# Kernel tuning notes

Measured on AMD Instinct MI355X. Metric: run time of the kernel, lower is better.

Reference implementation:

```python
import jax, jax.numpy as jnp
import numpy as np

D = 256; H = 8; L = 4; K = 4; AS = 2; HD = D // H
KK = K * K
LEVEL_SHAPES = [(128, 128), (64, 64), (32, 32), (16, 16)]


def _kernel_indices():
    # kernel_size=4 (even): linspace(-1.5, 1.5, 4); stack [j, i] then / K
    idx = jnp.linspace(-1.5, 1.5, K)
    ii, jj = jnp.meshgrid(idx, idx, indexing='ij')
    return jnp.stack([jj, ii], axis=-1).reshape(-1, 2) / K  # (KK, 2)


def _bilinear(vf, g, Hl, Wl):
    # vf: (b, H, Hl*Wl, HD) per-level value; g: (b, l1, H, KK, 2) in [0,1]
    # grid_sample semantics, align_corners=False, zero padding
    b, l1, h, kk, _ = g.shape
    x = g[..., 0] * Wl - 0.5
    y = g[..., 1] * Hl - 0.5
    x0 = jnp.floor(x)
    y0 = jnp.floor(y)
    acc = None
    for dx, dy in ((0, 0), (1, 0), (0, 1), (1, 1)):
        xi = x0 + dx
        yi = y0 + dy
        w = (1.0 - jnp.abs(x - xi)) * (1.0 - jnp.abs(y - yi))
        valid = (xi >= 0) & (xi < Wl) & (yi >= 0) & (yi < Hl)
        idx = (jnp.clip(yi, 0, Hl - 1) * Wl + jnp.clip(xi, 0, Wl - 1)).astype(jnp.int32)
        idx = idx.transpose(0, 2, 1, 3).reshape(b, h, l1 * kk)
        gth = jnp.take_along_axis(vf, idx[..., None], axis=2)  # (b,H,l1*kk,HD)
        ww = (w * valid).transpose(0, 2, 1, 3).reshape(b, h, l1 * kk)
        c = gth * ww[..., None]
        acc = c if acc is None else acc + c
    return acc.reshape(b, h, l1, kk, HD).transpose(0, 2, 1, 3, 4)  # (b,l1,H,kk,HD)


def setup_inputs() -> dict:
    key = jax.random.key(0)
    ks = jax.random.split(key, 9)
    b, l1 = 4, 1024
    l2 = sum(h * w for h, w in LEVEL_SHAPES)  # 21760
    query = jax.random.normal(ks[0], (b, l1, D), jnp.float32)
    value = jax.random.normal(ks[1], (b, l2, D), jnp.float32)
    centers = jax.random.uniform(ks[2], (b, l1, 2), jnp.float32)
    sizes = jax.random.uniform(ks[3], (b, l1, 2), jnp.float32) * 0.2 + 0.05
    ref_windows = jnp.concatenate([centers, sizes], axis=-1)  # (b,l1,4) cx,cy,w,h
    s = 1.0 / np.sqrt(D)
    Wv = jax.random.normal(ks[4], (D, D), jnp.float32) * s
    bv = jnp.zeros((D,), jnp.float32)
    Wo = jax.random.normal(ks[5], (D, D), jnp.float32) * s
    bo = jnp.zeros((D,), jnp.float32)
    Wbox = jax.random.normal(ks[6], (L * H * 4, D), jnp.float32) * 0.01
    bbox = jax.random.uniform(ks[7], (H * L * 4,), jnp.float32)
    Wattn = jax.random.normal(ks[8], (H * L * AS * AS, D), jnp.float32) * s
    battn = jnp.zeros((H * L * AS * AS,), jnp.float32)
    v_shape = np.array(LEVEL_SHAPES, np.int64)
    starts = np.cumsum([0] + [h * w for h, w in LEVEL_SHAPES[:-1]])
    v_start_index = np.array(starts, np.int64)
    v_mask = jnp.zeros((b, l2), bool)
    return dict(query=query, value=value, ref_windows=ref_windows, Wv=Wv, bv=bv,
                Wo=Wo, bo=bo, Wbox=Wbox, bbox=bbox, Wattn=Wattn, battn=battn,
                v_shape=v_shape, v_start_index=v_start_index, v_mask=v_mask)


def reference(query, value, ref_windows, Wv, bv, Wo, bo, Wbox, bbox, Wattn, battn,
              v_shape, v_start_index, v_mask):
    b, l1, _ = query.shape
    l2 = value.shape[1]
    # value projection + padding mask
    v = value @ Wv.T + bv
    v = jnp.where(v_mask[..., None], 0.0, v).reshape(b, l2, H, HD)
    # where to attend: offset boxes -> sampling grid (normalizer=None branch)
    off = (query @ Wbox.T + bbox).reshape(b, l1, H, L, 4)
    refw = ref_windows[:, :, None, None, :]            # (b,l1,1,1,4)
    refsz = jnp.concatenate([refw[..., 2:4], refw[..., 2:4]], axis=-1)
    boxes = refw + off / 8.0 * refsz                   # (b,l1,H,L,4)
    center = boxes[..., None, :2]
    size = boxes[..., None, 2:]
    grid = center + _kernel_indices() * jax.nn.relu(size)  # (b,l1,H,L,KK,2)
    # attention weights (attn_size grid upsampled to kernel_size by repeat_interleave)
    aw = (query @ Wattn.T + battn).reshape(b, l1, H, L, AS, AS)
    nr = K // AS
    aw = jnp.repeat(jnp.repeat(aw, nr, axis=-1), nr, axis=-2)  # (b,l1,H,L,K,K)
    sw = jax.nn.softmax(aw.reshape(b, l1, H, -1), axis=-1).reshape(b, l1, H, L, KK)
    lw = jax.nn.softmax(aw, axis=3).reshape(b, l1, H, L, KK)
    out = jnp.zeros((b, l1, H, HD), query.dtype)
    mout = jnp.zeros((b, l1, H, HD), query.dtype)
    for li in range(L):
        Hl, Wl = int(v_shape[li, 0]), int(v_shape[li, 1])
        st = int(v_start_index[li])
        vf = v[:, st:st + Hl * Wl].transpose(0, 2, 1, 3)  # (b,H,Hl*Wl,HD)
        samp = _bilinear(vf, grid[:, :, :, li], Hl, Wl)   # (b,l1,H,KK,HD)
        out = out + jnp.einsum('bqhkd,bqhk->bqhd', samp, sw[:, :, :, li])
        mout = mout + jnp.einsum('bqhkd,bqhk->bqhd', samp, lw[:, :, :, li])
    out = out.reshape(b, l1, D) @ Wo.T + bo
    mout = mout.reshape(b, l1, D) @ Wo.T + bo
    return out, mout, aw
```

## Files before the change

### kernel.cpp

```cpp
#include <hip/hip_runtime.h>
#include <hip/hip_bf16.h>


typedef __attribute__((ext_vector_type(8))) short short8;
typedef __attribute__((ext_vector_type(4))) float f32x4;
typedef __attribute__((ext_vector_type(4))) unsigned int uint4v;

__device__ __forceinline__ unsigned short f2bf(float f) {
    unsigned int u = __float_as_uint(f);
    unsigned int r = u + 0x7FFFu + ((u >> 16) & 1u);
    return (unsigned short)(r >> 16);
}
__device__ __forceinline__ unsigned int pkbf(float a, float b) {
    __hip_bfloat162 h = __float22bfloat162_rn(float2{a, b});
    return *reinterpret_cast<unsigned int*>(&h);
}
__device__ __forceinline__ short8 pack2(float4 x, float4 y) {
    uint4v u;
    u[0] = pkbf(x.x, x.y); u[1] = pkbf(x.z, x.w);
    u[2] = pkbf(y.x, y.y); u[3] = pkbf(y.z, y.w);
    return __builtin_bit_cast(short8, u);
}

__device__ __forceinline__ void storeC(float* C, size_t i, float v) { C[i] = v; }
__device__ __forceinline__ void storeC(unsigned short* C, size_t i, float v) { C[i] = f2bf(v); }

template <typename OutT>
__device__ __forceinline__ void gemm_body3(
    const float* __restrict__ A, const float* __restrict__ W,
    const float* __restrict__ bias, OutT* __restrict__ C,
    int N, int bm, int bn, char* smem)
{
    const int tid  = threadIdx.x;
    const int lane = tid & 63;
    const int wave = tid >> 6;
    const int wm = (wave & 1) * 64;
    const int wn = (wave >> 1) * 64;
    const int kg = lane >> 4;
    const int lm = lane & 15;

    char* ldsA = smem;
    char* ldsW = smem + 16384;

    f32x4 acc[4][4];
#pragma unroll
    for (int i = 0; i < 4; ++i)
#pragma unroll
        for (int j = 0; j < 4; ++j) {
            acc[i][j][0] = 0.f; acc[i][j][1] = 0.f;
            acc[i][j][2] = 0.f; acc[i][j][3] = 0.f;
        }

    const int prow = tid >> 1;
    const int ph   = tid & 1;
    const float* Ag = A + (size_t)(bm + prow) * 256 + ph * 16;
    const float* Wg = W + (size_t)(bn + prow) * 256 + ph * 16;
    const int f   = (prow >> 1) & 3;
    const int pp  = ph ^ (f >> 1);
    const int wlo = (f & 1) * 16;
    const int whi = wlo ^ 16;
    char* wA = ldsA + prow * 64 + pp * 32;
    char* wW = ldsW + prow * 64 + pp * 32;

    const int aslot = (kg ^ ((lm >> 1) & 3)) * 16;
    const int aoff  = (wm + lm) * 64 + aslot;
    const int woff  = (wn + lm) * 64 + aslot;

    float4 fa[4], fw[4];
#define ISSUE_VQ(K0)                                          \
    {                                                         \
        _Pragma("unroll")                                     \
        for (int q = 0; q < 4; ++q) {                         \
            fa[q] = *(const float4*)(Ag + (K0) + 4 * q);      \
            fw[q] = *(const float4*)(Wg + (K0) + 4 * q);      \
        }                                                     \
    }

    ISSUE_VQ(0)

    for (int it = 0; it < 8; ++it) {
        const int b = it & 1;
        char* wAb = wA + b * 8192;
        char* wWb = wW + b * 8192;
        *(short8*)(wAb + wlo) = pack2(fa[0], fa[1]);
        *(short8*)(wAb + whi) = pack2(fa[2], fa[3]);
        *(short8*)(wWb + wlo) = pack2(fw[0], fw[1]);
        *(short8*)(wWb + whi) = pack2(fw[2], fw[3]);
        __syncthreads();
        if (it < 7) ISSUE_VQ(32 * (it + 1))
        const char* bA = ldsA + b * 8192;
        const char* bW = ldsW + b * 8192;
        short8 af[4];
#pragma unroll
        for (int i = 0; i < 4; ++i)
            af[i] = *(const short8*)(bA + aoff + i * 1024);
#pragma unroll
        for (int j = 0; j < 4; ++j) {
            short8 bf = *(const short8*)(bW + woff + j * 1024);
#pragma unroll
            for (int i = 0; i < 4; ++i)
                acc[i][j] = __builtin_amdgcn_mfma_f32_16x16x32_bf16(
                    af[i], bf, acc[i][j], 0, 0, 0);
        }
    }
#undef ISSUE_VQ

#pragma unroll
    for (int j = 0; j < 4; ++j) {
        int col = bn + wn + j * 16 + lm;
        float bcol = bias[col];
#pragma unroll
        for (int i = 0; i < 4; ++i) {
#pragma unroll
            for (int r = 0; r < 4; ++r) {
                int row = bm + wm + i * 16 + kg * 4 + r;
                storeC(C, (size_t)row * N + col, acc[i][j][r] + bcol);
            }
        }
    }
}

#define LDA 56

__device__ __forceinline__ void gemm_body_f32(
    const float* __restrict__ A, const float* __restrict__ W,
    const float* __restrict__ bias, float* __restrict__ C,
    int N, int bm, int bn, unsigned short* As, unsigned short* Ws)
{
    const int tid  = threadIdx.x;
    const int lane = tid & 63;
    const int wave = tid >> 6;
    const int wm = (wave & 1) * 64;
    const int wn = (wave >> 1) * 64;
    const int lr = tid >> 1;
    const int lh = (tid & 1) * 16;
    const int kg = lane >> 4;
    const int lm = lane & 15;

    f32x4 acc[4][4];
#pragma unroll
    for (int i = 0; i < 4; ++i)
#pragma unroll
        for (int j = 0; j < 4; ++j) {
            acc[i][j][0] = 0.f; acc[i][j][1] = 0.f;
            acc[i][j][2] = 0.f; acc[i][j][3] = 0.f;
        }

    const float* Ap = A + (size_t)(bm + lr) * 256 + lh;
    const float* Wp = W + (size_t)(bn + lr) * 256 + lh;
    unsigned short* Asp = &As[lr * LDA + lh];
    unsigned short* Wsp = &Ws[lr * LDA + lh];

    for (int k0 = 0; k0 < 256; k0 += 32) {
        float4 a0 = *(const float4*)(Ap + k0);
        float4 a1 = *(const float4*)(Ap + k0 + 4);
        float4 a2 = *(const float4*)(Ap + k0 + 8);
        float4 a3 = *(const float4*)(Ap + k0 + 12);
        float4 w0 = *(const float4*)(Wp + k0);
        float4 w1 = *(const float4*)(Wp + k0 + 4);
        float4 w2 = *(const float4*)(Wp + k0 + 8);
        float4 w3 = *(const float4*)(Wp + k0 + 12);
        __syncthreads();
        *(short8*)(Asp)     = pack2(a0, a1);
        *(short8*)(Asp + 8) = pack2(a2, a3);
        *(short8*)(Wsp)     = pack2(w0, w1);
        *(short8*)(Wsp + 8) = pack2(w2, w3);
        __syncthreads();
        short8 af[4], bfr[4];
#pragma unroll
        for (int i = 0; i < 4; ++i)
            af[i] = *(const short8*)&As[(wm + i * 16 + lm) * LDA + kg * 8];
#pragma unroll
        for (int j = 0; j < 4; ++j)
            bfr[j] = *(const short8*)&Ws[(wn + j * 16 + lm) * LDA + kg * 8];
#pragma unroll
        for (int i = 0; i < 4; ++i)
#pragma unroll
            for (int j = 0; j < 4; ++j)
                acc[i][j] = __builtin_amdgcn_mfma_f32_16x16x32_bf16(
                    af[i], bfr[j], acc[i][j], 0, 0, 0);
    }

#pragma unroll
    for (int j = 0; j < 4; ++j) {
        int col = bn + wn + j * 16 + lm;
        float bcol = bias[col];
#pragma unroll
        for (int i = 0; i < 4; ++i)
#pragma unroll
            for (int r = 0; r < 4; ++r) {
                int row = bm + wm + i * 16 + kg * 4 + r;
                C[(size_t)row * N + col] = acc[i][j][r] + bcol;
            }
    }
}

__device__ __forceinline__ void gemm_body_bf16A(
    const unsigned short* __restrict__ A, const float* __restrict__ W,
    const float* __restrict__ bias, float* __restrict__ C,
    int N, int bm, int bn, unsigned short* As, unsigned short* Ws)
{
    const int tid  = threadIdx.x;
    const int lane = tid & 63;
    const int wave = tid >> 6;
    const int wm = (wave & 1) * 64;
    const int wn = (wave >> 1) * 64;
    const int lr = tid >> 1;
    const int lh = (tid & 1) * 16;
    const int kg = lane >> 4;
    const int lm = lane & 15;

    f32x4 acc[4][4];
#pragma unroll
    for (int i = 0; i < 4; ++i)
#pragma unroll
        for (int j = 0; j < 4; ++j) {
            acc[i][j][0] = 0.f; acc[i][j][1] = 0.f;
            acc[i][j][2] = 0.f; acc[i][j][3] = 0.f;
        }

    const unsigned short* Ap = A + (size_t)(bm + lr) * 256 + lh;
    const float* Wp = W + (size_t)(bn + lr) * 256 + lh;
    unsigned short* Asp = &As[lr * LDA + lh];
    unsigned short* Wsp = &Ws[lr * LDA + lh];

    for (int k0 = 0; k0 < 256; k0 += 32) {
        uint4v a01 = *(const uint4v*)(Ap + k0);
        uint4v a23 = *(const uint4v*)(Ap + k0 + 8);
        float4 w0 = *(const float4*)(Wp + k0);
        float4 w1 = *(const float4*)(Wp + k0 + 4);
        float4 w2 = *(const float4*)(Wp + k0 + 8);
        float4 w3 = *(const float4*)(Wp + k0 + 12);
        __syncthreads();
        *(short8*)(Asp)     = __builtin_bit_cast(short8, a01);
        *(short8*)(Asp + 8) = __builtin_bit_cast(short8, a23);
        *(short8*)(Wsp)     = pack2(w0, w1);
        *(short8*)(Wsp + 8) = pack2(w2, w3);
        __syncthreads();
        short8 af[4], bfr[4];
#pragma unroll
        for (int i = 0; i < 4; ++i)
            af[i] = *(const short8*)&As[(wm + i * 16 + lm) * LDA + kg * 8];
#pragma unroll
        for (int j = 0; j < 4; ++j)
            bfr[j] = *(const short8*)&Ws[(wn + j * 16 + lm) * LDA + kg * 8];
#pragma unroll
        for (int i = 0; i < 4; ++i)
#pragma unroll
            for (int j = 0; j < 4; ++j)
                acc[i][j] = __builtin_amdgcn_mfma_f32_16x16x32_bf16(
                    af[i], bfr[j], acc[i][j], 0, 0, 0);
    }

#pragma unroll
    for (int j = 0; j < 4; ++j) {
        int col = bn + wn + j * 16 + lm;
        float bcol = bias[col];
#pragma unroll
        for (int i = 0; i < 4; ++i)
#pragma unroll
            for (int r = 0; r < 4; ++r) {
                int row = bm + wm + i * 16 + kg * 4 + r;
                C[(size_t)row * N + col] = acc[i][j][r] + bcol;
            }
    }
}

__global__ __launch_bounds__(256, 4) void gemm_vq_kernel(
    const float* __restrict__ value, const float* __restrict__ Wv,
    const float* __restrict__ bv, unsigned short* __restrict__ v,
    const float* __restrict__ query,
    const float* __restrict__ Wbox, const float* __restrict__ bbox, float* __restrict__ off,
    const float* __restrict__ Wattn, const float* __restrict__ battn, float* __restrict__ awr)
{
    __shared__ __align__(16) char smem[32768];
    const int x = blockIdx.x;
    if (x < 1360) {
        gemm_body3<unsigned short>(value, Wv, bv, v, 256,
                                   (x >> 1) * 128, (x & 1) * 128, smem);
    } else {
        const int idx = x - 1360;
        const int bm = (idx & 31) * 128;
        unsigned short* As = (unsigned short*)smem;
        unsigned short* Ws = As + 128 * LDA;
        if (idx < 32) gemm_body_f32(query, Wbox, bbox, off, 128, bm, 0, As, Ws);
        else          gemm_body_f32(query, Wattn, battn, awr, 128, bm, 0, As, Ws);
    }
}

__global__ __launch_bounds__(256) void gemm_o_kernel(
    const unsigned short* __restrict__ A, const float* __restrict__ W,
    const float* __restrict__ bias, float* __restrict__ C)
{
    __shared__ __align__(16) unsigned short As[128 * LDA];
    __shared__ __align__(16) unsigned short Ws[128 * LDA];
    gemm_body_bf16A(A, W, bias, C, 256, blockIdx.x * 128, blockIdx.y * 128, As, Ws);
}

__global__ __launch_bounds__(512, 8) void sample_kernel(
    const unsigned short* __restrict__ v, const float* __restrict__ off,
    const float* __restrict__ awr, const float* __restrict__ refw,
    float* __restrict__ aw_out, unsigned short* __restrict__ accb)
{
    const int x  = blockIdx.x;
    const int bq = ((x & 3) << 10) | (x >> 2);
    const int b  = bq >> 10;
    const int t  = threadIdx.x;

    __shared__ float ref4[4];
    __shared__ float awl[128];
    __shared__ float bxs[128];
    __shared__ float swl[512];
    __shared__ float lwl[512];
    __shared__ int4  tp[32 * 66];

    if (t < 4)   ref4[t] = refw[bq * 4 + t];
    if (t < 128) awl[t] = awr[(size_t)bq * 128 + t];
    __syncthreads();

    if (t < 128) {
        float o = off[(size_t)bq * 128 + t];
        int comp = t & 3;
        float r0 = ref4[0], r1 = ref4[1], r2 = ref4[2], r3 = ref4[3];
        float bx;
        if (comp == 0)      bx = r0 + o * 0.125f * r2;
        else if (comp == 1) bx = r1 + o * 0.125f * r3;
        else if (comp == 2) bx = r2 + o * 0.125f * r2;
        else                bx = r3 + o * 0.125f * r3;
        bxs[t] = bx;

        const int h = t >> 4, r = t & 15;
        float a = awl[t];
        float m = a;
#pragma unroll
        for (int s = 1; s < 16; s <<= 1) m = fmaxf(m, __shfl_xor(m, s, 16));
        float se = expf(a - m);
#pragma unroll
        for (int s = 1; s < 16; s <<= 1) se += __shfl_xor(se, s, 16);
        const float inv_s = 1.0f / (4.0f * se);

        float* awq = aw_out + (size_t)bq * 512 + h * 64;
#pragma unroll
        for (int j = 0; j < 4; ++j) {
            int eidx = r * 4 + j;
            int l  = eidx >> 4;
            int ky = (eidx >> 2) & 3;
            int kx = eidx & 3;
            int pos = (ky >> 1) * 2 + (kx >> 1);
            float raw = awl[h * 16 + l * 4 + pos];
            swl[h * 64 + eidx] = expf(raw - m) * inv_s;
            int base = h * 16 + pos;
            float m2 = awl[base];
#pragma unroll
            for (int li = 1; li < 4; ++li) m2 = fmaxf(m2, awl[base + li * 4]);
            float s2 = 0.f;
#pragma unroll
            for (int li = 0; li < 4; ++li) s2 += expf(awl[base + li * 4] - m2);
            lwl[h * 64 + eidx] = expf(raw - m2) / s2;
            awq[eidx] = raw;
        }
    }
    __syncthreads();

    {
        const int STs_[4] = {0, 16384, 20480, 21504};
        int e = t;
        int eh = e >> 6, rem = e & 63, l = rem >> 4, kk = rem & 15;
        const float* bx = &bxs[eh * 16 + l * 4];
        float cx = bx[0], cy = bx[1];
        float bw = fmaxf(bx[2], 0.f), bh = fmaxf(bx[3], 0.f);
        float kx = -0.375f + 0.25f * (float)(kk & 3);
        float ky = -0.375f + 0.25f * (float)(kk >> 2);
        int Wl = 128 >> l;
        float xg = (cx + kx * bw) * (float)Wl - 0.5f;
        float yg = (cy + ky * bh) * (float)Wl - 0.5f;
        float x0f = floorf(xg), y0f = floorf(yg);
        int x0 = (int)x0f, y0 = (int)y0f;
        float fx = xg - x0f, fy = yg - y0f;
        float sww = swl[e], lww = lwl[e];
        int rowbase = b * 21760 + STs_[l];
        int4* dst = &tp[(eh * 4 + l) * 66 + kk * 4];
#pragma unroll
        for (int tap = 0; tap < 4; ++tap) {
            int dx = tap & 1, dy = tap >> 1;
            int xi = x0 + dx, yi = y0 + dy;
            float w = (dx ? fx : 1.f - fx) * (dy ? fy : 1.f - fy);
            if (xi < 0 || xi >= Wl || yi < 0 || yi >= Wl) w = 0.f;
            int xc = min(max(xi, 0), Wl - 1);
            int yc = min(max(yi, 0), Wl - 1);
            dst[tap] = int4{(rowbase + yc * Wl + xc) << 6,
                            __float_as_int(w * sww),
                            __float_as_int(w * lww), 0};
        }
    }
    __syncthreads();

    const int h    = t >> 6;
    const int lane = t & 63;
    const int l    = (lane >> 4) & 3;
    const int sub  = (lane >> 3) & 1;
    const int cl   = lane & 7;
    const uint2* vp = (const uint2*)v;
    const int choff = h * 8 + cl;
    const int4* sp = &tp[(h * 4 + l) * 66 + sub];

    float a0 = 0.f, a1 = 0.f, a2 = 0.f, a3 = 0.f;
    float m0 = 0.f, m1 = 0.f, m2 = 0.f, m3 = 0.f;
#pragma unroll 4
    for (int i = 0; i < 32; ++i) {
        int4 d = sp[2 * i];
        uint2 pv = vp[(size_t)(d.x + choff)];
        float v0 = __uint_as_float(pv.x << 16);
        float v1 = __uint_as_float(pv.x & 0xffff0000u);
        float v2 = __uint_as_float(pv.y << 16);
        float v3 = __uint_as_float(pv.y & 0xffff0000u);
        float wo = __int_as_float(d.y), wm = __int_as_float(d.z);
        a0 = fmaf(v0, wo, a0); a1 = fmaf(v1, wo, a1);
        a2 = fmaf(v2, wo, a2); a3 = fmaf(v3, wo, a3);
        m0 = fmaf(v0, wm, m0); m1 = fmaf(v1, wm, m1);
        m2 = fmaf(v2, wm, m2); m3 = fmaf(v3, wm, m3);
    }
#pragma unroll
    for (int s = 8; s <= 32; s <<= 1) {
        a0 += __shfl_xor(a0, s); a1 += __shfl_xor(a1, s);
        a2 += __shfl_xor(a2, s); a3 += __shfl_xor(a3, s);
        m0 += __shfl_xor(m0, s); m1 += __shfl_xor(m1, s);
        m2 += __shfl_xor(m2, s); m3 += __shfl_xor(m3, s);
    }
    if (lane < 8) {
        size_t base = (size_t)bq * 256 + h * 32 + cl * 4;
        *(uint2*)&accb[base] = uint2{pkbf(a0, a1), pkbf(a2, a3)};
        *(uint2*)&accb[base + (size_t)4096 * 256] = uint2{pkbf(m0, m1), pkbf(m2, m3)};
    }
}

extern "C" void kernel_launch(void* const* d_in, const int* in_sizes, int n_in,
                              void* d_out, int out_size, void* d_ws, size_t ws_size,
                              hipStream_t stream) {
    const float* query = (const float*)d_in[0];
    const float* value = (const float*)d_in[1];
    const float* refw  = (const float*)d_in[2];
    const float* Wv    = (const float*)d_in[3];
    const float* bv    = (const float*)d_in[4];
    const float* Wo    = (const float*)d_in[5];
    const float* bo    = (const float*)d_in[6];
    const float* Wbox  = (const float*)d_in[7];
    const float* bbox  = (const float*)d_in[8];
    const float* Wattn = (const float*)d_in[9];
    const float* battn = (const float*)d_in[10];

    float* out = (float*)d_out;
    float* aw_out = out + 2 * 1048576;

    unsigned short* v = (unsigned short*)d_ws;
    float* off = (float*)((char*)d_ws + 44564480);
    float* awr = off + 524288;
    unsigned short* accb = (unsigned short*)(awr + 524288);

    gemm_vq_kernel<<<1424, 256, 0, stream>>>(value, Wv, bv, v,
                                             query, Wbox, bbox, off,
                                             Wattn, battn, awr);
    sample_kernel<<<4096, 512, 0, stream>>>(v, off, awr, refw, aw_out, accb);
    gemm_o_kernel<<<dim3(64, 2), 256, 0, stream>>>(accb, Wo, bo, out);
}
```

Before: 250.2 us.

## Deepen global-load prefetch to two stages in value-projection GEMM

The value-projection GEMM body now keeps two register stages of float4 loads in flight, issuing loads for k-step it+2 while packing the data for step it. The full __syncthreads is replaced by an LDS-only waitcnt plus s_barrier, so outstanding global loads are not drained at each barrier. The K loop is fully unrolled and the min-blocks launch bound is dropped to give the compiler register room for the extra stage. The aim is to hide global memory latency behind MFMA work, at the cost of higher register pressure and possibly lower occupancy.

```diff
diff --git a/kernel.cpp b/kernel.cpp
--- a/kernel.cpp
+++ b/kernel.cpp
@@ -26,7 +26,7 @@
 __device__ __forceinline__ void storeC(unsigned short* C, size_t i, float v) { C[i] = f2bf(v); }
 
 template <typename OutT>
-__device__ __forceinline__ void gemm_body3(
+__device__ __forceinline__ void gemm_body4(
     const float* __restrict__ A, const float* __restrict__ W,
     const float* __restrict__ bias, OutT* __restrict__ C,
     int N, int bm, int bn, char* smem)
@@ -66,30 +66,36 @@
     const int aoff  = (wm + lm) * 64 + aslot;
     const int woff  = (wn + lm) * 64 + aslot;
 
-    float4 fa[4], fw[4];
-#define ISSUE_VQ(K0)                                          \
-    {                                                         \
-        _Pragma("unroll")                                     \
-        for (int q = 0; q < 4; ++q) {                         \
-            fa[q] = *(const float4*)(Ag + (K0) + 4 * q);      \
-            fw[q] = *(const float4*)(Wg + (K0) + 4 * q);      \
-        }                                                     \
-    }
-
-    ISSUE_VQ(0)
-
+    float4 fa[2][4], fw[2][4];
+#pragma unroll
+    for (int s = 0; s < 2; ++s)
+#pragma unroll
+        for (int q = 0; q < 4; ++q) {
+            fa[s][q] = *(const float4*)(Ag + 32 * s + 4 * q);
+            fw[s][q] = *(const float4*)(Wg + 32 * s + 4 * q);
+        }
+
+#pragma unroll
     for (int it = 0; it < 8; ++it) {
-        const int b = it & 1;
-        char* wAb = wA + b * 8192;
-        char* wWb = wW + b * 8192;
-        *(short8*)(wAb + wlo) = pack2(fa[0], fa[1]);
-        *(short8*)(wAb + whi) = pack2(fa[2], fa[3]);
-        *(short8*)(wWb + wlo) = pack2(fw[0], fw[1]);
-        *(short8*)(wWb + whi) = pack2(fw[2], fw[3]);
-        __syncthreads();
-        if (it < 7) ISSUE_VQ(32 * (it + 1))
-        const char* bA = ldsA + b * 8192;
-        const char* bW = ldsW + b * 8192;
+        const int s = it & 1;
+        char* wAb = wA + s * 8192;
+        char* wWb = wW + s * 8192;
+        *(short8*)(wAb + wlo) = pack2(fa[s][0], fa[s][1]);
+        *(short8*)(wAb + whi) = pack2(fa[s][2], fa[s][3]);
+        *(short8*)(wWb + wlo) = pack2(fw[s][0], fw[s][1]);
+        *(short8*)(wWb + whi) = pack2(fw[s][2], fw[s][3]);
+        if (it < 6) {
+            const int k0 = 32 * (it + 2);
+#pragma unroll
+            for (int q = 0; q < 4; ++q) {
+                fa[s][q] = *(const float4*)(Ag + k0 + 4 * q);
+                fw[s][q] = *(const float4*)(Wg + k0 + 4 * q);
+            }
+        }
+        asm volatile("s_waitcnt lgkmcnt(0)" ::: "memory");
+        __builtin_amdgcn_s_barrier();
+        const char* bA = ldsA + s * 8192;
+        const char* bW = ldsW + s * 8192;
         short8 af[4];
 #pragma unroll
         for (int i = 0; i < 4; ++i)
@@ -103,7 +109,6 @@
                     af[i], bf, acc[i][j], 0, 0, 0);
         }
     }
-#undef ISSUE_VQ
 
 #pragma unroll
     for (int j = 0; j < 4; ++j) {
@@ -266,7 +271,7 @@
     }
 }
 
-__global__ __launch_bounds__(256, 4) void gemm_vq_kernel(
+__global__ __launch_bounds__(256) void gemm_vq_kernel(
     const float* __restrict__ value, const float* __restrict__ Wv,
     const float* __restrict__ bv, unsigned short* __restrict__ v,
     const float* __restrict__ query,
@@ -276,7 +281,7 @@
     __shared__ __align__(16) char smem[32768];
     const int x = blockIdx.x;
     if (x < 1360) {
-        gemm_body3<unsigned short>(value, Wv, bv, v, 256,
+        gemm_body4<unsigned short>(value, Wv, bv, v, 256,
                                    (x >> 1) * 128, (x & 1) * 128, smem);
     } else {
         const int idx = x - 1360;
```

Measured after the change: 252.8 us. No clear change (+1.0%).
